# Kernel optimization log

Hardware: AMD Instinct MI355X
Metric: run time of the kernel (lower is better)

Reference implementation:

```python
import math
import jax, jax.numpy as jnp
import numpy as np

CHUNK_LEN = 64
NUM_HEADS = 16
HIDDEN = 1024
HEAD = HIDDEN // NUM_HEADS


def setup_inputs() -> dict:
    key = jax.random.key(0)
    ks = jax.random.split(key, 8)
    B, S, C, N, L = 4, 2048, 32, 2, 128
    scale = 1.0 / math.sqrt(HIDDEN)
    return {
        "query": jax.random.normal(ks[0], (B, S, HIDDEN), jnp.float32),
        "kv": jax.random.normal(ks[1], (B, C, N, L, HIDDEN), jnp.float32),
        "Wq": jax.random.normal(ks[2], (HIDDEN, HIDDEN), jnp.float32) * scale,
        "bq": jnp.zeros((HIDDEN,), jnp.float32),
        "Wk": jax.random.normal(ks[3], (HIDDEN, HIDDEN), jnp.float32) * scale,
        "bk": jnp.zeros((HIDDEN,), jnp.float32),
        "Wv": jax.random.normal(ks[4], (HIDDEN, HIDDEN), jnp.float32) * scale,
        "bv": jnp.zeros((HIDDEN,), jnp.float32),
    }


def reference(query, kv, Wq, bq, Wk, bk, Wv, bv):
    B, S, H = query.shape
    _, C, N, L, _ = kv.shape
    # shift query right by chunk_len-1 and pad to n_chunks*chunk_len
    q = query[:, CHUNK_LEN - 1:]
    add_len = C * CHUNK_LEN - q.shape[1]
    q = jnp.pad(q, ((0, 0), (0, add_len), (0, 0)))
    q = q.reshape(B, C, CHUNK_LEN, H)
    q = (q @ Wq.T + bq).reshape(B, C, CHUNK_LEN, NUM_HEADS, HEAD)
    k = (kv @ Wk.T + bk).reshape(B, C, N, L, NUM_HEADS, HEAD)
    v = (kv @ Wv.T + bv).reshape(B, C, N, L, NUM_HEADS, HEAD)
    # scores: [B, C, heads, chunk_len, N, L]
    attn = jnp.einsum("bcihd,bcnjhd->bchinj", q, k) / math.sqrt(HEAD)
    # softmax over flattened neighbor dims (n, j)
    attn = jax.nn.softmax(attn.reshape(B, C, NUM_HEADS, CHUNK_LEN, N * L), axis=-1)
    attn = attn.reshape(B, C, NUM_HEADS, CHUNK_LEN, N, L)
    h = jnp.einsum("bchinj,bcnjhd->bcihd", attn, v).reshape(B, C * CHUNK_LEN, H)
    # shift left: prepend chunk_len-1 zeros, truncate to seq_len
    h = jnp.pad(h, ((0, 0), (CHUNK_LEN - 1, 0), (0, 0)))[:, :S]
    return h
```

## Files before the change

### kernel.cpp

```cpp
#include <hip/hip_runtime.h>
#include <stdint.h>

#define HD 1024
#define SEQ 2048
#define NC 32

typedef __bf16 bf16x4 __attribute__((ext_vector_type(4)));
typedef __bf16 bf16x8 __attribute__((ext_vector_type(8)));
typedef float f32x4 __attribute__((ext_vector_type(4)));

__device__ inline unsigned short f2bf(float f) {
  union { float f; unsigned int u; } v; v.f = f;
  unsigned int r = v.u + 0x7fffu + ((v.u >> 16) & 1u);
  return (unsigned short)(r >> 16);
}
__device__ inline unsigned int pk2bf(float a, float b) {
  return (unsigned int)f2bf(a) | ((unsigned int)f2bf(b) << 16);
}
__device__ inline bf16x8 ld_frag8(const unsigned short* p) {
  bf16x4 lo = *(const bf16x4*)p;
  bf16x4 hi = *(const bf16x4*)(p + 4);
  return __builtin_shufflevector(lo, hi, 0, 1, 2, 3, 4, 5, 6, 7);
}
__device__ inline void glds16(const unsigned short* g, unsigned short* l) {
  __builtin_amdgcn_global_load_lds(
      (const __attribute__((address_space(1))) unsigned int*)g,
      (__attribute__((address_space(3))) unsigned int*)l, 16, 0, 0);
}
__device__ inline int2 swz_bid() {
  int lin = blockIdx.y * 8 + blockIdx.x;
  int s = (lin & 7) * (int)gridDim.y + (lin >> 3);
  return make_int2(s & 7, s >> 3);
}
__device__ inline int swz64(int row, int j) { return (row * 8 + (j ^ (row & 7))) * 8; }
__device__ inline int swz32(int row, int j) {
  int lr8 = row >> 1;
  return (lr8 * 8 + ((((row & 1) << 2) | j) ^ (lr8 & 7))) * 8;
}

__global__ __launch_bounds__(256) void zero_head_kernel(float* __restrict__ out) {
  int i = (blockIdx.x * 256 + threadIdx.x) * 4;
  int b = i / 64512;
  int r = i - b * 64512;
  *(float4*)(out + (size_t)b * (SEQ * HD) + r) = make_float4(0.f, 0.f, 0.f, 0.f);
}

__global__ __launch_bounds__(256) void prep_q_kernel(const float* __restrict__ q,
                                                     unsigned short* __restrict__ out,
                                                     float* __restrict__ oz) {
  int bid = blockIdx.x;
  if (bid < 252) {
    int i = (bid * 256 + threadIdx.x) * 4;
    int b = i / 64512;
    int r = i - b * 64512;
    *(float4*)(oz + (size_t)b * (SEQ * HD) + r) = make_float4(0.f, 0.f, 0.f, 0.f);
    return;
  }
  int i = (bid - 252) * 256 + threadIdx.x;
  int g = i >> 7, c8 = (i & 127) * 8;
  int b = g >> 11, tt = g & 2047;
  uint4 o = make_uint4(0, 0, 0, 0);
  if (tt < 1985) {
    const float* src = q + ((size_t)(b << 11) + tt + 63) * HD + c8;
    float4 a = *(const float4*)src;
    float4 bb = *(const float4*)(src + 4);
    o = make_uint4(pk2bf(a.x, a.y), pk2bf(a.z, a.w), pk2bf(bb.x, bb.y), pk2bf(bb.z, bb.w));
  }
  *(uint4*)(out + (size_t)g * HD + c8) = o;
}

__global__ __launch_bounds__(256) void cvt_kernel(const float* __restrict__ in,
                                                  unsigned short* __restrict__ out, int n8) {
  int i = blockIdx.x * 256 + threadIdx.x;
  if (i < n8) {
    float4 a = ((const float4*)in)[(size_t)i * 2];
    float4 b = ((const float4*)in)[(size_t)i * 2 + 1];
    ((uint4*)out)[i] = make_uint4(pk2bf(a.x, a.y), pk2bf(a.z, a.w),
                                  pk2bf(b.x, b.y), pk2bf(b.z, b.w));
  }
}

__global__ __launch_bounds__(256) void cvt_w3_kernel(const float* __restrict__ Wq,
                                                     const float* __restrict__ Wk,
                                                     const float* __restrict__ Wv,
                                                     unsigned short* __restrict__ dst) {
  int bid = blockIdx.x;
  int which = bid >> 9;
  int i = (bid & 511) * 256 + threadIdx.x;
  const float* src = which == 0 ? Wq : (which == 1 ? Wk : Wv);
  float4 a = ((const float4*)src)[(size_t)i * 2];
  float4 b = ((const float4*)src)[(size_t)i * 2 + 1];
  ((uint4*)(dst + (size_t)which * 1048576))[i] =
      make_uint4(pk2bf(a.x, a.y), pk2bf(a.z, a.w), pk2bf(b.x, b.y), pk2bf(b.z, b.w));
}

__global__ __launch_bounds__(256, 2) void gemm_q_kernel(
    const unsigned short* __restrict__ A, const unsigned short* __restrict__ W,
    const float* __restrict__ bias, unsigned short* __restrict__ Cout) {
  __shared__ unsigned short lds_a[128 * 64];
  __shared__ unsigned short lds_b[128 * 64];
  const int t = threadIdx.x;
  const int l = t & 63, w = t >> 6;
  const int wm = w >> 1, wn = w & 1;
  const int lr = l & 15, lq = l >> 4;
  const int2 bid = swz_bid();
  const size_t arow0 = (size_t)bid.y * 128;
  const size_t brow0 = (size_t)bid.x * 128;
  int pr[4], pco[4];
#pragma unroll
  for (int p = 0; p < 4; ++p) {
    int pc = p * 256 + t;
    pr[p] = pc >> 3;
    pco[p] = ((pc & 7) ^ (pr[p] & 7)) * 8;
  }

  f32x4 acc[4][4];
  for (int i = 0; i < 4; i++)
    for (int j = 0; j < 4; j++) acc[i][j] = (f32x4){0.f, 0.f, 0.f, 0.f};

  for (int kk = 0; kk < 16; ++kk) {
    const int k0 = kk * 64;
    __syncthreads();
#pragma unroll
    for (int p = 0; p < 4; ++p) {
      glds16(A + (arow0 + pr[p]) * HD + k0 + pco[p], lds_a + (p * 256 + t) * 8);
      glds16(W + (brow0 + pr[p]) * HD + k0 + pco[p], lds_b + (p * 256 + t) * 8);
    }
    __syncthreads();
#pragma unroll
    for (int h = 0; h < 2; ++h) {
      bf16x8 af[4], bfr[4];
      for (int mt = 0; mt < 4; ++mt)
        af[mt] = *(const bf16x8*)(lds_a + swz64(wm * 64 + mt * 16 + lr, h * 4 + lq));
      for (int nt = 0; nt < 4; ++nt)
        bfr[nt] = *(const bf16x8*)(lds_b + swz64(wn * 64 + nt * 16 + lr, h * 4 + lq));
      for (int mt = 0; mt < 4; ++mt)
        for (int nt = 0; nt < 4; ++nt)
          acc[mt][nt] = __builtin_amdgcn_mfma_f32_16x16x32_bf16(af[mt], bfr[nt], acc[mt][nt], 0, 0, 0);
    }
  }

  for (int nt = 0; nt < 4; ++nt) {
    int n = bid.x * 128 + wn * 64 + nt * 16 + lr;
    float bvv = bias[n];
    for (int mt = 0; mt < 4; ++mt) {
      size_t mbase = arow0 + wm * 64 + mt * 16 + lq * 4;
      for (int r = 0; r < 4; ++r)
        Cout[(mbase + r) * HD + n] = f2bf(acc[mt][nt][r] + bvv);
    }
  }
}

__global__ __launch_bounds__(256, 2) void gemm_kv_kernel(
    const unsigned short* __restrict__ A, const unsigned short* __restrict__ Wk,
    const unsigned short* __restrict__ Wv, const float* __restrict__ bk,
    const float* __restrict__ bv, unsigned short* __restrict__ Kout,
    unsigned short* __restrict__ Vt) {
  __shared__ unsigned short lds_a[2][128 * 32];
  __shared__ unsigned short lds_k[2][128 * 32];
  __shared__ unsigned short lds_v[2][128 * 32];
  const int t = threadIdx.x;
  const int l = t & 63, w = t >> 6;
  const int wm = w >> 1, wn = w & 1;
  const int lr = l & 15, lq = l >> 4;
  const int2 bid = swz_bid();
  const size_t arow0 = (size_t)bid.y * 128;
  const size_t brow0 = (size_t)bid.x * 128;
  int pr[2], pco[2];
#pragma unroll
  for (int p = 0; p < 2; ++p) {
    int pc = p * 256 + t;
    int lr8 = pc >> 3;
    int e = (pc & 7) ^ (lr8 & 7);
    pr[p] = lr8 * 2 + (e >> 2);
    pco[p] = (e & 3) * 8;
  }

  f32x4 acck[4][4], accv[4][4];
  for (int i = 0; i < 4; i++)
    for (int j = 0; j < 4; j++) {
      acck[i][j] = (f32x4){0.f, 0.f, 0.f, 0.f};
      accv[i][j] = (f32x4){0.f, 0.f, 0.f, 0.f};
    }

  auto stage = [&](int buf, int k0) {
#pragma unroll
    for (int p = 0; p < 2; ++p) {
      glds16(A + (arow0 + pr[p]) * HD + k0 + pco[p], lds_a[buf] + (p * 256 + t) * 8);
      glds16(Wk + (brow0 + pr[p]) * HD + k0 + pco[p], lds_k[buf] + (p * 256 + t) * 8);
      glds16(Wv + (brow0 + pr[p]) * HD + k0 + pco[p], lds_v[buf] + (p * 256 + t) * 8);
    }
  };
  auto compute = [&](int buf) {
    bf16x8 af[4];
    for (int mt = 0; mt < 4; ++mt)
      af[mt] = *(const bf16x8*)(lds_a[buf] + swz32(wm * 64 + mt * 16 + lr, lq));
    {
      bf16x8 bfr[4];
      for (int nt = 0; nt < 4; ++nt)
        bfr[nt] = *(const bf16x8*)(lds_k[buf] + swz32(wn * 64 + nt * 16 + lr, lq));
      for (int mt = 0; mt < 4; ++mt)
        for (int nt = 0; nt < 4; ++nt)
          acck[mt][nt] = __builtin_amdgcn_mfma_f32_16x16x32_bf16(af[mt], bfr[nt], acck[mt][nt], 0, 0, 0);
    }
    {
      bf16x8 bfr[4];
      for (int nt = 0; nt < 4; ++nt)
        bfr[nt] = *(const bf16x8*)(lds_v[buf] + swz32(wn * 64 + nt * 16 + lr, lq));
      for (int mt = 0; mt < 4; ++mt)
        for (int nt = 0; nt < 4; ++nt)
          accv[mt][nt] = __builtin_amdgcn_mfma_f32_16x16x32_bf16(af[mt], bfr[nt], accv[mt][nt], 0, 0, 0);
    }
  };

  stage(0, 0);
  for (int kk = 0; kk < 31; ++kk) {
    const int cur = kk & 1;
    stage(cur ^ 1, (kk + 1) * 32);
    asm volatile("s_waitcnt vmcnt(6)" ::: "memory");
    __builtin_amdgcn_s_barrier();
    compute(cur);
    __builtin_amdgcn_s_barrier();
  }
  asm volatile("s_waitcnt vmcnt(0)" ::: "memory");
  __builtin_amdgcn_s_barrier();
  compute(1);

  for (int nt = 0; nt < 4; ++nt) {
    int n = bid.x * 128 + wn * 64 + nt * 16 + lr;
    float bvv = bk[n];
    for (int mt = 0; mt < 4; ++mt) {
      size_t mbase = arow0 + wm * 64 + mt * 16 + lq * 4;
      for (int r = 0; r < 4; ++r)
        Kout[(mbase + r) * HD + n] = f2bf(acck[mt][nt][r] + bvv);
    }
  }
  for (int nt = 0; nt < 4; ++nt) {
    int n = bid.x * 128 + wn * 64 + nt * 16 + lr;
    float bvv = bv[n];
    int h = n >> 6, d = n & 63;
    for (int mt = 0; mt < 4; ++mt) {
      size_t m0 = arow0 + wm * 64 + mt * 16 + lq * 4;
      size_t bc = m0 >> 8, j = m0 & 255;
      *(ushort4*)(Vt + ((bc * 16 + h) * 64 + d) * 256 + j) =
          make_ushort4(f2bf(accv[mt][nt][0] + bvv), f2bf(accv[mt][nt][1] + bvv),
                       f2bf(accv[mt][nt][2] + bvv), f2bf(accv[mt][nt][3] + bvv));
    }
  }
}

__global__ __launch_bounds__(256, 2) void gemm_f32_kernel(
    const float* __restrict__ A, const float* __restrict__ W,
    const float* __restrict__ bias, unsigned short* __restrict__ Cout,
    int store_vt, int qremap) {
  __shared__ unsigned short lds_a[128 * 32];
  __shared__ unsigned short lds_b[128 * 32];
  const int t = threadIdx.x;
  const int l = t & 63, w = t >> 6;
  const int wm = w >> 1, wn = w & 1;
  const int lr = l & 15, lq = l >> 4;
  const size_t arow0 = (size_t)blockIdx.y * 128;
  const size_t brow0 = (size_t)blockIdx.x * 128;

  f32x4 acc[4][4];
  for (int i = 0; i < 4; i++)
    for (int j = 0; j < 4; j++) acc[i][j] = (f32x4){0.f, 0.f, 0.f, 0.f};

  for (int kk = 0; kk < 32; ++kk) {
    const int k0 = kk * 32;
    uint4 av[2], bv[2];
    for (int p = 0; p < 2; ++p) {
      int chunk = p * 256 + t;
      int row = chunk >> 2, c8 = (chunk & 3) * 8;
      size_t grow = arow0 + row;
      bool valid = true;
      const float* srcA;
      if (qremap) {
        int bb = (int)(grow >> 11), tt = (int)(grow & 2047);
        valid = tt < 1985;
        srcA = A + ((size_t)(bb << 11) + tt + 63) * HD + k0 + c8;
      } else {
        srcA = A + grow * HD + k0 + c8;
      }
      if (valid) {
        float4 x = *(const float4*)srcA, y = *(const float4*)(srcA + 4);
        av[p] = make_uint4(pk2bf(x.x, x.y), pk2bf(x.z, x.w), pk2bf(y.x, y.y), pk2bf(y.z, y.w));
      } else av[p] = make_uint4(0, 0, 0, 0);
      const float* srcB = W + (brow0 + row) * HD + k0 + c8;
      float4 x = *(const float4*)srcB, y = *(const float4*)(srcB + 4);
      bv[p] = make_uint4(pk2bf(x.x, x.y), pk2bf(x.z, x.w), pk2bf(y.y, y.y), pk2bf(y.z, y.w));
    }
    for (int p = 0; p < 2; ++p) {
      int chunk = p * 256 + t;
      int row = chunk >> 2, c8 = (chunk & 3) * 8;
      const float* srcB = W + (brow0 + row) * HD + k0 + c8;
      float4 x = *(const float4*)srcB, y = *(const float4*)(srcB + 4);
      bv[p] = make_uint4(pk2bf(x.x, x.y), pk2bf(x.z, x.w), pk2bf(y.x, y.y), pk2bf(y.z, y.w));
    }
    __syncthreads();
    for (int p = 0; p < 2; ++p) {
      int chunk = p * 256 + t;
      *(uint4*)(lds_a + chunk * 8) = av[p];
      *(uint4*)(lds_b + chunk * 8) = bv[p];
    }
    __syncthreads();
    bf16x8 af[4], bfr[4];
    for (int mt = 0; mt < 4; ++mt)
      af[mt] = *(const bf16x8*)(lds_a + (wm * 64 + mt * 16 + lr) * 32 + lq * 8);
    for (int nt = 0; nt < 4; ++nt)
      bfr[nt] = *(const bf16x8*)(lds_b + (wn * 64 + nt * 16 + lr) * 32 + lq * 8);
    for (int mt = 0; mt < 4; ++mt)
      for (int nt = 0; nt < 4; ++nt)
        acc[mt][nt] = __builtin_amdgcn_mfma_f32_16x16x32_bf16(af[mt], bfr[nt], acc[mt][nt], 0, 0, 0);
  }

  if (!store_vt) {
    for (int nt = 0; nt < 4; ++nt) {
      int n = blockIdx.x * 128 + wn * 64 + nt * 16 + lr;
      float bvv = bias[n];
      for (int mt = 0; mt < 4; ++mt) {
        size_t mbase = arow0 + wm * 64 + mt * 16 + lq * 4;
        for (int r = 0; r < 4; ++r)
          Cout[(mbase + r) * HD + n] = f2bf(acc[mt][nt][r] + bvv);
      }
    }
  } else {
    for (int nt = 0; nt < 4; ++nt) {
      int n = blockIdx.x * 128 + wn * 64 + nt * 16 + lr;
      float bvv = bias[n];
      int h = n >> 6, d = n & 63;
      for (int mt = 0; mt < 4; ++mt) {
        size_t m0 = arow0 + wm * 64 + mt * 16 + lq * 4;
        size_t bc = m0 >> 8, j = m0 & 255;
        *(ushort4*)(Cout + ((bc * 16 + h) * 64 + d) * 256 + j) =
            make_ushort4(f2bf(acc[mt][nt][0] + bvv), f2bf(acc[mt][nt][1] + bvv),
                         f2bf(acc[mt][nt][2] + bvv), f2bf(acc[mt][nt][3] + bvv));
      }
    }
  }
}

#define QK_STRIDE 72
#define P_STRIDE 260

__global__ __launch_bounds__(256, 3) void attn_kernel(
    const unsigned short* __restrict__ Qp, const unsigned short* __restrict__ Kp,
    const unsigned short* __restrict__ Vt, float* __restrict__ out) {
  __shared__ unsigned short k_s[256 * QK_STRIDE];
  const int t = threadIdx.x;
  const int l = t & 63, w = t >> 6;
  const int lr = l & 15, lq = l >> 4;
  const int bid = blockIdx.x;
  const int head = bid & 15, cc = (bid >> 4) & 31, b = bid >> 9;
  const size_t qrow0 = (size_t)(b * NC + cc) * 64;
  const size_t kvrow0 = (size_t)(b * NC + cc) * 256;
  const int hcol = head * 64;
  const unsigned short* vbase = Vt + ((size_t)((b * NC + cc) * 16 + head) * 64) * 256;

  for (int p = 0; p < 8; ++p) {
    int chunk = p * 256 + t;
    int row = chunk >> 3, c8 = (chunk & 7) * 8;
    *(uint4*)(k_s + row * QK_STRIDE + c8) = *(const uint4*)(Kp + (kvrow0 + row) * HD + hcol + c8);
  }
  bf16x8 qa0 = ld_frag8(Qp + (qrow0 + w * 16 + lr) * HD + hcol + lq * 8);
  bf16x8 qa1 = ld_frag8(Qp + (qrow0 + w * 16 + lr) * HD + hcol + 32 + lq * 8);
  __syncthreads();

  f32x4 sc[16];
  __builtin_amdgcn_s_setprio(1);
  for (int nt = 0; nt < 16; ++nt) {
    bf16x8 kb0 = ld_frag8(k_s + (nt * 16 + lr) * QK_STRIDE + lq * 8);
    bf16x8 kb1 = ld_frag8(k_s + (nt * 16 + lr) * QK_STRIDE + 32 + lq * 8);
    f32x4 a = (f32x4){0.f, 0.f, 0.f, 0.f};
    a = __builtin_amdgcn_mfma_f32_16x16x32_bf16(kb0, qa0, a, 0, 0, 0);
    a = __builtin_amdgcn_mfma_f32_16x16x32_bf16(kb1, qa1, a, 0, 0, 0);
    sc[nt] = a;
  }
  __builtin_amdgcn_s_setprio(0);

  float m = -1e30f;
  for (int nt = 0; nt < 16; ++nt)
    for (int r = 0; r < 4; ++r) m = fmaxf(m, sc[nt][r]);
  m = fmaxf(m, __shfl_xor(m, 16));
  m = fmaxf(m, __shfl_xor(m, 32));
  float s = 0.f;
  const float cexp = 0.18033688011112042f;
  for (int nt = 0; nt < 16; ++nt)
    for (int r = 0; r < 4; ++r) {
      float p = exp2f((sc[nt][r] - m) * cexp);
      sc[nt][r] = p;
      s += p;
    }
  s += __shfl_xor(s, 16);
  s += __shfl_xor(s, 32);

  bf16x8 va[4];
#pragma unroll
  for (int nt2 = 0; nt2 < 4; ++nt2)
    va[nt2] = *(const bf16x8*)(vbase + (size_t)(nt2 * 16 + lr) * 256 + lq * 8);

  __syncthreads();

  for (int nt = 0; nt < 16; ++nt) {
    *(uint2*)(k_s + (w * 16 + lr) * P_STRIDE + nt * 16 + lq * 4) =
        make_uint2(pk2bf(sc[nt][0], sc[nt][1]), pk2bf(sc[nt][2], sc[nt][3]));
  }

  f32x4 o[4];
  for (int i = 0; i < 4; ++i) o[i] = (f32x4){0.f, 0.f, 0.f, 0.f};
  bf16x8 vbuf[4];
#pragma unroll
  for (int ks = 0; ks < 8; ks += 2) {
#pragma unroll
    for (int nt2 = 0; nt2 < 4; ++nt2)
      vbuf[nt2] = *(const bf16x8*)(vbase + (size_t)(nt2 * 16 + lr) * 256 + (ks + 1) * 32 + lq * 8);
    bf16x8 pa = ld_frag8(k_s + (w * 16 + lr) * P_STRIDE + ks * 32 + lq * 8);
    __builtin_amdgcn_s_setprio(1);
#pragma unroll
    for (int nt2 = 0; nt2 < 4; ++nt2)
      o[nt2] = __builtin_amdgcn_mfma_f32_16x16x32_bf16(pa, va[nt2], o[nt2], 0, 0, 0);
    __builtin_amdgcn_s_setprio(0);
    if (ks + 2 < 8) {
#pragma unroll
      for (int nt2 = 0; nt2 < 4; ++nt2)
        va[nt2] = *(const bf16x8*)(vbase + (size_t)(nt2 * 16 + lr) * 256 + (ks + 2) * 32 + lq * 8);
    }
    bf16x8 pb = ld_frag8(k_s + (w * 16 + lr) * P_STRIDE + (ks + 1) * 32 + lq * 8);
    __builtin_amdgcn_s_setprio(1);
#pragma unroll
    for (int nt2 = 0; nt2 < 4; ++nt2)
      o[nt2] = __builtin_amdgcn_mfma_f32_16x16x32_bf16(pb, vbuf[nt2], o[nt2], 0, 0, 0);
    __builtin_amdgcn_s_setprio(0);
  }

  for (int r = 0; r < 4; ++r) {
    int strip = w * 16 + lq * 4 + r;
    int trow = cc * 64 + strip;
    float sv = __shfl(s, lq * 4 + r, 16);
    if (trow < 1985) {
      size_t orow = (size_t)b * SEQ + trow + 63;
      float inv = 1.0f / sv;
      for (int nt2 = 0; nt2 < 4; ++nt2)
        out[orow * HD + hcol + nt2 * 16 + lr] = o[nt2][r] * inv;
    }
  }
}

extern "C" void kernel_launch(void* const* d_in, const int* in_sizes, int n_in,
                              void* d_out, int out_size, void* d_ws, size_t ws_size,
                              hipStream_t stream) {
  (void)in_sizes; (void)n_in; (void)out_size;
  const float* query = (const float*)d_in[0];
  const float* kv    = (const float*)d_in[1];
  const float* Wq    = (const float*)d_in[2];
  const float* bq    = (const float*)d_in[3];
  const float* Wk    = (const float*)d_in[4];
  const float* bk    = (const float*)d_in[5];
  const float* Wv    = (const float*)d_in[6];
  const float* bv    = (const float*)d_in[7];
  float* out = (float*)d_out;

  unsigned short* Qp  = (unsigned short*)d_ws;
  unsigned short* Kp  = Qp + (size_t)8192 * 1024;
  unsigned short* Vt  = Kp + (size_t)32768 * 1024;
  unsigned short* Qbf = Vt + (size_t)32768 * 1024;
  unsigned short* KVb = Qbf + (size_t)8192 * 1024;
  unsigned short* Wqb = KVb + (size_t)32768 * 1024;
  const size_t need = ((size_t)8192 * 1024 * 2 + (size_t)32768 * 1024 * 2 + (size_t)1024 * 1024 * 3) * 2;
  const bool big = ws_size >= need;

  if (big) {
    prep_q_kernel<<<dim3(4348), dim3(256), 0, stream>>>(query, Qbf, out);
    cvt_w3_kernel<<<dim3(1536), dim3(256), 0, stream>>>(Wq, Wk, Wv, Wqb);
    cvt_kernel<<<dim3(16384), dim3(256), 0, stream>>>(kv, KVb, 4194304);
    gemm_q_kernel<<<dim3(8, 64), dim3(256), 0, stream>>>(Qbf, Wqb, bq, Qp);
    gemm_kv_kernel<<<dim3(8, 256), dim3(256), 0, stream>>>(KVb, Wqb + (size_t)1048576,
                                                           Wqb + (size_t)2097152, bk, bv, Kp, Vt);
  } else {
    zero_head_kernel<<<dim3(252), dim3(256), 0, stream>>>(out);
    gemm_f32_kernel<<<dim3(8, 64), dim3(256), 0, stream>>>(query, Wq, bq, Qp, 0, 1);
    gemm_f32_kernel<<<dim3(8, 256), dim3(256), 0, stream>>>(kv, Wk, bk, Kp, 0, 0);
    gemm_f32_kernel<<<dim3(8, 256), dim3(256), 0, stream>>>(kv, Wv, bv, Vt, 1, 0);
  }
  attn_kernel<<<dim3(2048), dim3(256), 0, stream>>>(Qp, Kp, Vt, out);
}
```

Baseline: 466.9 us.

## Merge conversion kernels and Q/KV projection GEMMs into single launches

```diff
diff --git a/kernel.cpp b/kernel.cpp
--- a/kernel.cpp
+++ b/kernel.cpp
@@ -27,16 +27,7 @@
       (const __attribute__((address_space(1))) unsigned int*)g,
       (__attribute__((address_space(3))) unsigned int*)l, 16, 0, 0);
 }
-__device__ inline int2 swz_bid() {
-  int lin = blockIdx.y * 8 + blockIdx.x;
-  int s = (lin & 7) * (int)gridDim.y + (lin >> 3);
-  return make_int2(s & 7, s >> 3);
-}
 __device__ inline int swz64(int row, int j) { return (row * 8 + (j ^ (row & 7))) * 8; }
-__device__ inline int swz32(int row, int j) {
-  int lr8 = row >> 1;
-  return (lr8 * 8 + ((((row & 1) << 2) | j) ^ (lr8 & 7))) * 8;
-}
 
 __global__ __launch_bounds__(256) void zero_head_kernel(float* __restrict__ out) {
   int i = (blockIdx.x * 256 + threadIdx.x) * 4;
@@ -45,67 +36,67 @@
   *(float4*)(out + (size_t)b * (SEQ * HD) + r) = make_float4(0.f, 0.f, 0.f, 0.f);
 }
 
-__global__ __launch_bounds__(256) void prep_q_kernel(const float* __restrict__ q,
-                                                     unsigned short* __restrict__ out,
-                                                     float* __restrict__ oz) {
+__global__ __launch_bounds__(256) void prep_all_kernel(
+    const float* __restrict__ query, const float* __restrict__ kv,
+    const float* __restrict__ Wq, const float* __restrict__ Wk,
+    const float* __restrict__ Wv, unsigned short* __restrict__ Qbf,
+    unsigned short* __restrict__ KVb, unsigned short* __restrict__ Wb,
+    float* __restrict__ oz) {
   int bid = blockIdx.x;
-  if (bid < 252) {
-    int i = (bid * 256 + threadIdx.x) * 4;
-    int b = i / 64512;
-    int r = i - b * 64512;
-    *(float4*)(oz + (size_t)b * (SEQ * HD) + r) = make_float4(0.f, 0.f, 0.f, 0.f);
+  if (bid < 16384) {
+    int i = bid * 256 + threadIdx.x;
+    float4 a = ((const float4*)kv)[(size_t)i * 2];
+    float4 b = ((const float4*)kv)[(size_t)i * 2 + 1];
+    ((uint4*)KVb)[i] = make_uint4(pk2bf(a.x, a.y), pk2bf(a.z, a.w),
+                                  pk2bf(b.x, b.y), pk2bf(b.z, b.w));
     return;
   }
-  int i = (bid - 252) * 256 + threadIdx.x;
-  int g = i >> 7, c8 = (i & 127) * 8;
-  int b = g >> 11, tt = g & 2047;
-  uint4 o = make_uint4(0, 0, 0, 0);
-  if (tt < 1985) {
-    const float* src = q + ((size_t)(b << 11) + tt + 63) * HD + c8;
-    float4 a = *(const float4*)src;
-    float4 bb = *(const float4*)(src + 4);
-    o = make_uint4(pk2bf(a.x, a.y), pk2bf(a.z, a.w), pk2bf(bb.x, bb.y), pk2bf(bb.z, bb.w));
-  }
-  *(uint4*)(out + (size_t)g * HD + c8) = o;
-}
-
-__global__ __launch_bounds__(256) void cvt_kernel(const float* __restrict__ in,
-                                                  unsigned short* __restrict__ out, int n8) {
-  int i = blockIdx.x * 256 + threadIdx.x;
-  if (i < n8) {
-    float4 a = ((const float4*)in)[(size_t)i * 2];
-    float4 b = ((const float4*)in)[(size_t)i * 2 + 1];
-    ((uint4*)out)[i] = make_uint4(pk2bf(a.x, a.y), pk2bf(a.z, a.w),
-                                  pk2bf(b.x, b.y), pk2bf(b.z, b.w));
-  }
-}
-
-__global__ __launch_bounds__(256) void cvt_w3_kernel(const float* __restrict__ Wq,
-                                                     const float* __restrict__ Wk,
-                                                     const float* __restrict__ Wv,
-                                                     unsigned short* __restrict__ dst) {
-  int bid = blockIdx.x;
-  int which = bid >> 9;
-  int i = (bid & 511) * 256 + threadIdx.x;
-  const float* src = which == 0 ? Wq : (which == 1 ? Wk : Wv);
-  float4 a = ((const float4*)src)[(size_t)i * 2];
-  float4 b = ((const float4*)src)[(size_t)i * 2 + 1];
-  ((uint4*)(dst + (size_t)which * 1048576))[i] =
-      make_uint4(pk2bf(a.x, a.y), pk2bf(a.z, a.w), pk2bf(b.x, b.y), pk2bf(b.z, b.w));
-}
-
-__global__ __launch_bounds__(256, 2) void gemm_q_kernel(
-    const unsigned short* __restrict__ A, const unsigned short* __restrict__ W,
-    const float* __restrict__ bias, unsigned short* __restrict__ Cout) {
+  bid -= 16384;
+  if (bid < 4096) {
+    int i = bid * 256 + threadIdx.x;
+    int g = i >> 7, c8 = (i & 127) * 8;
+    int b = g >> 11, tt = g & 2047;
+    uint4 o = make_uint4(0, 0, 0, 0);
+    if (tt < 1985) {
+      const float* src = query + ((size_t)(b << 11) + tt + 63) * HD + c8;
+      float4 a = *(const float4*)src;
+      float4 bb = *(const float4*)(src + 4);
+      o = make_uint4(pk2bf(a.x, a.y), pk2bf(a.z, a.w), pk2bf(bb.x, bb.y), pk2bf(bb.z, bb.w));
+    }
+    *(uint4*)(Qbf + (size_t)g * HD + c8) = o;
+    return;
+  }
+  bid -= 4096;
+  if (bid < 1536) {
+    int which = bid >> 9;
+    int i = (bid & 511) * 256 + threadIdx.x;
+    const float* src = which == 0 ? Wq : (which == 1 ? Wk : Wv);
+    float4 a = ((const float4*)src)[(size_t)i * 2];
+    float4 b = ((const float4*)src)[(size_t)i * 2 + 1];
+    ((uint4*)(Wb + (size_t)which * 1048576))[i] =
+        make_uint4(pk2bf(a.x, a.y), pk2bf(a.z, a.w), pk2bf(b.x, b.y), pk2bf(b.z, b.w));
+    return;
+  }
+  bid -= 1536;
+  int i = (bid * 256 + threadIdx.x) * 4;
+  int b = i / 64512;
+  int r = i - b * 64512;
+  *(float4*)(oz + (size_t)b * (SEQ * HD) + r) = make_float4(0.f, 0.f, 0.f, 0.f);
+}
+
+__global__ __launch_bounds__(256, 2) void gemm_all_kernel(
+    const unsigned short* __restrict__ Qbf, const unsigned short* __restrict__ KVb,
+    const unsigned short* __restrict__ Wb,
+    const float* __restrict__ bq, const float* __restrict__ bk, const float* __restrict__ bv,
+    unsigned short* __restrict__ Qp, unsigned short* __restrict__ Kp,
+    unsigned short* __restrict__ Vt) {
   __shared__ unsigned short lds_a[128 * 64];
   __shared__ unsigned short lds_b[128 * 64];
+  __shared__ unsigned short lds_c[128 * 64];
   const int t = threadIdx.x;
   const int l = t & 63, w = t >> 6;
   const int wm = w >> 1, wn = w & 1;
   const int lr = l & 15, lq = l >> 4;
-  const int2 bid = swz_bid();
-  const size_t arow0 = (size_t)bid.y * 128;
-  const size_t brow0 = (size_t)bid.x * 128;
   int pr[4], pco[4];
 #pragma unroll
   for (int p = 0; p < 4; ++p) {
@@ -114,137 +105,118 @@
     pco[p] = ((pc & 7) ^ (pr[p] & 7)) * 8;
   }
 
-  f32x4 acc[4][4];
-  for (int i = 0; i < 4; i++)
-    for (int j = 0; j < 4; j++) acc[i][j] = (f32x4){0.f, 0.f, 0.f, 0.f};
-
-  for (int kk = 0; kk < 16; ++kk) {
-    const int k0 = kk * 64;
-    __syncthreads();
-#pragma unroll
-    for (int p = 0; p < 4; ++p) {
-      glds16(A + (arow0 + pr[p]) * HD + k0 + pco[p], lds_a + (p * 256 + t) * 8);
-      glds16(W + (brow0 + pr[p]) * HD + k0 + pco[p], lds_b + (p * 256 + t) * 8);
-    }
-    __syncthreads();
-#pragma unroll
-    for (int h = 0; h < 2; ++h) {
-      bf16x8 af[4], bfr[4];
-      for (int mt = 0; mt < 4; ++mt)
-        af[mt] = *(const bf16x8*)(lds_a + swz64(wm * 64 + mt * 16 + lr, h * 4 + lq));
-      for (int nt = 0; nt < 4; ++nt)
-        bfr[nt] = *(const bf16x8*)(lds_b + swz64(wn * 64 + nt * 16 + lr, h * 4 + lq));
-      for (int mt = 0; mt < 4; ++mt)
+  if (blockIdx.y < 256) {
+    int lin = blockIdx.y * 8 + blockIdx.x;
+    int s = (lin & 7) * 256 + (lin >> 3);
+    const int bx = s & 7, by = s >> 3;
+    const size_t arow0 = (size_t)by * 128;
+    const size_t brow0 = (size_t)bx * 128;
+    const unsigned short* Wk = Wb + (size_t)1048576;
+    const unsigned short* Wv = Wb + (size_t)2097152;
+
+    f32x4 acck[4][4], accv[4][4];
+    for (int i = 0; i < 4; i++)
+      for (int j = 0; j < 4; j++) {
+        acck[i][j] = (f32x4){0.f, 0.f, 0.f, 0.f};
+        accv[i][j] = (f32x4){0.f, 0.f, 0.f, 0.f};
+      }
+
+    for (int kk = 0; kk < 16; ++kk) {
+      const int k0 = kk * 64;
+      __syncthreads();
+#pragma unroll
+      for (int p = 0; p < 4; ++p) {
+        glds16(KVb + (arow0 + pr[p]) * HD + k0 + pco[p], lds_a + (p * 256 + t) * 8);
+        glds16(Wk + (brow0 + pr[p]) * HD + k0 + pco[p], lds_b + (p * 256 + t) * 8);
+        glds16(Wv + (brow0 + pr[p]) * HD + k0 + pco[p], lds_c + (p * 256 + t) * 8);
+      }
+      __syncthreads();
+#pragma unroll
+      for (int h = 0; h < 2; ++h) {
+        bf16x8 af[4];
+        for (int mt = 0; mt < 4; ++mt)
+          af[mt] = *(const bf16x8*)(lds_a + swz64(wm * 64 + mt * 16 + lr, h * 4 + lq));
+        {
+          bf16x8 bfr[4];
+          for (int nt = 0; nt < 4; ++nt)
+            bfr[nt] = *(const bf16x8*)(lds_b + swz64(wn * 64 + nt * 16 + lr, h * 4 + lq));
+          for (int mt = 0; mt < 4; ++mt)
+            for (int nt = 0; nt < 4; ++nt)
+              acck[mt][nt] = __builtin_amdgcn_mfma_f32_16x16x32_bf16(af[mt], bfr[nt], acck[mt][nt], 0, 0, 0);
+        }
+        {
+          bf16x8 bfr[4];
+          for (int nt = 0; nt < 4; ++nt)
+            bfr[nt] = *(const bf16x8*)(lds_c + swz64(wn * 64 + nt * 16 + lr, h * 4 + lq));
+          for (int mt = 0; mt < 4; ++mt)
+            for (int nt = 0; nt < 4; ++nt)
+              accv[mt][nt] = __builtin_amdgcn_mfma_f32_16x16x32_bf16(af[mt], bfr[nt], accv[mt][nt], 0, 0, 0);
+        }
+      }
+    }
+
+    for (int nt = 0; nt < 4; ++nt) {
+      int n = bx * 128 + wn * 64 + nt * 16 + lr;
+      float bvv = bk[n];
+      for (int mt = 0; mt < 4; ++mt) {
+        size_t mbase = arow0 + wm * 64 + mt * 16 + lq * 4;
+        for (int r = 0; r < 4; ++r)
+          Kp[(mbase + r) * HD + n] = f2bf(acck[mt][nt][r] + bvv);
+      }
+    }
+    for (int nt = 0; nt < 4; ++nt) {
+      int n = bx * 128 + wn * 64 + nt * 16 + lr;
+      float bvv = bv[n];
+      int h = n >> 6, d = n & 63;
+      for (int mt = 0; mt < 4; ++mt) {
+        size_t m0 = arow0 + wm * 64 + mt * 16 + lq * 4;
+        size_t bc = m0 >> 8, j = m0 & 255;
+        *(ushort4*)(Vt + ((bc * 16 + h) * 64 + d) * 256 + j) =
+            make_ushort4(f2bf(accv[mt][nt][0] + bvv), f2bf(accv[mt][nt][1] + bvv),
+                         f2bf(accv[mt][nt][2] + bvv), f2bf(accv[mt][nt][3] + bvv));
+      }
+    }
+  } else {
+    int lin = (blockIdx.y - 256) * 8 + blockIdx.x;
+    int s = (lin & 7) * 64 + (lin >> 3);
+    const int bx = s & 7, by = s >> 3;
+    const size_t arow0 = (size_t)by * 128;
+    const size_t brow0 = (size_t)bx * 128;
+
+    f32x4 acc[4][4];
+    for (int i = 0; i < 4; i++)
+      for (int j = 0; j < 4; j++) acc[i][j] = (f32x4){0.f, 0.f, 0.f, 0.f};
+
+    for (int kk = 0; kk < 16; ++kk) {
+      const int k0 = kk * 64;
+      __syncthreads();
+#pragma unroll
+      for (int p = 0; p < 4; ++p) {
+        glds16(Qbf + (arow0 + pr[p]) * HD + k0 + pco[p], lds_a + (p * 256 + t) * 8);
+        glds16(Wb + (brow0 + pr[p]) * HD + k0 + pco[p], lds_b + (p * 256 + t) * 8);
+      }
+      __syncthreads();
+#pragma unroll
+      for (int h = 0; h < 2; ++h) {
+        bf16x8 af[4], bfr[4];
+        for (int mt = 0; mt < 4; ++mt)
+          af[mt] = *(const bf16x8*)(lds_a + swz64(wm * 64 + mt * 16 + lr, h * 4 + lq));
         for (int nt = 0; nt < 4; ++nt)
-          acc[mt][nt] = __builtin_amdgcn_mfma_f32_16x16x32_bf16(af[mt], bfr[nt], acc[mt][nt], 0, 0, 0);
-    }
-  }
-
-  for (int nt = 0; nt < 4; ++nt) {
-    int n = bid.x * 128 + wn * 64 + nt * 16 + lr;
-    float bvv = bias[n];
-    for (int mt = 0; mt < 4; ++mt) {
-      size_t mbase = arow0 + wm * 64 + mt * 16 + lq * 4;
-      for (int r = 0; r < 4; ++r)
-        Cout[(mbase + r) * HD + n] = f2bf(acc[mt][nt][r] + bvv);
-    }
-  }
-}
-
-__global__ __launch_bounds__(256, 2) void gemm_kv_kernel(
-    const unsigned short* __restrict__ A, const unsigned short* __restrict__ Wk,
-    const unsigned short* __restrict__ Wv, const float* __restrict__ bk,
-    const float* __restrict__ bv, unsigned short* __restrict__ Kout,
-    unsigned short* __restrict__ Vt) {
-  __shared__ unsigned short lds_a[2][128 * 32];
-  __shared__ unsigned short lds_k[2][128 * 32];
-  __shared__ unsigned short lds_v[2][128 * 32];
-  const int t = threadIdx.x;
-  const int l = t & 63, w = t >> 6;
-  const int wm = w >> 1, wn = w & 1;
-  const int lr = l & 15, lq = l >> 4;
-  const int2 bid = swz_bid();
-  const size_t arow0 = (size_t)bid.y * 128;
-  const size_t brow0 = (size_t)bid.x * 128;
-  int pr[2], pco[2];
-#pragma unroll
-  for (int p = 0; p < 2; ++p) {
-    int pc = p * 256 + t;
-    int lr8 = pc >> 3;
-    int e = (pc & 7) ^ (lr8 & 7);
-    pr[p] = lr8 * 2 + (e >> 2);
-    pco[p] = (e & 3) * 8;
-  }
-
-  f32x4 acck[4][4], accv[4][4];
-  for (int i = 0; i < 4; i++)
-    for (int j = 0; j < 4; j++) {
-      acck[i][j] = (f32x4){0.f, 0.f, 0.f, 0.f};
-      accv[i][j] = (f32x4){0.f, 0.f, 0.f, 0.f};
-    }
-
-  auto stage = [&](int buf, int k0) {
-#pragma unroll
-    for (int p = 0; p < 2; ++p) {
-      glds16(A + (arow0 + pr[p]) * HD + k0 + pco[p], lds_a[buf] + (p * 256 + t) * 8);
-      glds16(Wk + (brow0 + pr[p]) * HD + k0 + pco[p], lds_k[buf] + (p * 256 + t) * 8);
-      glds16(Wv + (brow0 + pr[p]) * HD + k0 + pco[p], lds_v[buf] + (p * 256 + t) * 8);
-    }
-  };
-  auto compute = [&](int buf) {
-    bf16x8 af[4];
-    for (int mt = 0; mt < 4; ++mt)
-      af[mt] = *(const bf16x8*)(lds_a[buf] + swz32(wm * 64 + mt * 16 + lr, lq));
-    {
-      bf16x8 bfr[4];
-      for (int nt = 0; nt < 4; ++nt)
-        bfr[nt] = *(const bf16x8*)(lds_k[buf] + swz32(wn * 64 + nt * 16 + lr, lq));
-      for (int mt = 0; mt < 4; ++mt)
-        for (int nt = 0; nt < 4; ++nt)
-          acck[mt][nt] = __builtin_amdgcn_mfma_f32_16x16x32_bf16(af[mt], bfr[nt], acck[mt][nt], 0, 0, 0);
-    }
-    {
-      bf16x8 bfr[4];
-      for (int nt = 0; nt < 4; ++nt)
-        bfr[nt] = *(const bf16x8*)(lds_v[buf] + swz32(wn * 64 + nt * 16 + lr, lq));
-      for (int mt = 0; mt < 4; ++mt)
-        for (int nt = 0; nt < 4; ++nt)
-          accv[mt][nt] = __builtin_amdgcn_mfma_f32_16x16x32_bf16(af[mt], bfr[nt], accv[mt][nt], 0, 0, 0);
-    }
-  };
-
-  stage(0, 0);
-  for (int kk = 0; kk < 31; ++kk) {
-    const int cur = kk & 1;
-    stage(cur ^ 1, (kk + 1) * 32);
-    asm volatile("s_waitcnt vmcnt(6)" ::: "memory");
-    __builtin_amdgcn_s_barrier();
-    compute(cur);
-    __builtin_amdgcn_s_barrier();
-  }
-  asm volatile("s_waitcnt vmcnt(0)" ::: "memory");
-  __builtin_amdgcn_s_barrier();
-  compute(1);
-
-  for (int nt = 0; nt < 4; ++nt) {
-    int n = bid.x * 128 + wn * 64 + nt * 16 + lr;
-    float bvv = bk[n];
-    for (int mt = 0; mt < 4; ++mt) {
-      size_t mbase = arow0 + wm * 64 + mt * 16 + lq * 4;
-      for (int r = 0; r < 4; ++r)
-        Kout[(mbase + r) * HD + n] = f2bf(acck[mt][nt][r] + bvv);
-    }
-  }
-  for (int nt = 0; nt < 4; ++nt) {
-    int n = bid.x * 128 + wn * 64 + nt * 16 + lr;
-    float bvv = bv[n];
-    int h = n >> 6, d = n & 63;
-    for (int mt = 0; mt < 4; ++mt) {
-      size_t m0 = arow0 + wm * 64 + mt * 16 + lq * 4;
-      size_t bc = m0 >> 8, j = m0 & 255;
-      *(ushort4*)(Vt + ((bc * 16 + h) * 64 + d) * 256 + j) =
-          make_ushort4(f2bf(accv[mt][nt][0] + bvv), f2bf(accv[mt][nt][1] + bvv),
-                       f2bf(accv[mt][nt][2] + bvv), f2bf(accv[mt][nt][3] + bvv));
+          bfr[nt] = *(const bf16x8*)(lds_b + swz64(wn * 64 + nt * 16 + lr, h * 4 + lq));
+        for (int mt = 0; mt < 4; ++mt)
+          for (int nt = 0; nt < 4; ++nt)
+            acc[mt][nt] = __builtin_amdgcn_mfma_f32_16x16x32_bf16(af[mt], bfr[nt], acc[mt][nt], 0, 0, 0);
+      }
+    }
+
+    for (int nt = 0; nt < 4; ++nt) {
+      int n = bx * 128 + wn * 64 + nt * 16 + lr;
+      float bvv = bq[n];
+      for (int mt = 0; mt < 4; ++mt) {
+        size_t mbase = arow0 + wm * 64 + mt * 16 + lq * 4;
+        for (int r = 0; r < 4; ++r)
+          Qp[(mbase + r) * HD + n] = f2bf(acc[mt][nt][r] + bvv);
+      }
     }
   }
 }
@@ -288,13 +260,6 @@
       } else av[p] = make_uint4(0, 0, 0, 0);
       const float* srcB = W + (brow0 + row) * HD + k0 + c8;
       float4 x = *(const float4*)srcB, y = *(const float4*)(srcB + 4);
-      bv[p] = make_uint4(pk2bf(x.x, x.y), pk2bf(x.z, x.w), pk2bf(y.y, y.y), pk2bf(y.z, y.w));
-    }
-    for (int p = 0; p < 2; ++p) {
-      int chunk = p * 256 + t;
-      int row = chunk >> 2, c8 = (chunk & 3) * 8;
-      const float* srcB = W + (brow0 + row) * HD + k0 + c8;
-      float4 x = *(const float4*)srcB, y = *(const float4*)(srcB + 4);
       bv[p] = make_uint4(pk2bf(x.x, x.y), pk2bf(x.z, x.w), pk2bf(y.x, y.y), pk2bf(y.z, y.w));
     }
     __syncthreads();
@@ -470,12 +435,10 @@
   const bool big = ws_size >= need;
 
   if (big) {
-    prep_q_kernel<<<dim3(4348), dim3(256), 0, stream>>>(query, Qbf, out);
-    cvt_w3_kernel<<<dim3(1536), dim3(256), 0, stream>>>(Wq, Wk, Wv, Wqb);
-    cvt_kernel<<<dim3(16384), dim3(256), 0, stream>>>(kv, KVb, 4194304);
-    gemm_q_kernel<<<dim3(8, 64), dim3(256), 0, stream>>>(Qbf, Wqb, bq, Qp);
-    gemm_kv_kernel<<<dim3(8, 256), dim3(256), 0, stream>>>(KVb, Wqb + (size_t)1048576,
-                                                           Wqb + (size_t)2097152, bk, bv, Kp, Vt);
+    prep_all_kernel<<<dim3(22268), dim3(256), 0, stream>>>(query, kv, Wq, Wk, Wv,
+                                                           Qbf, KVb, Wqb, out);
+    gemm_all_kernel<<<dim3(8, 320), dim3(256), 0, stream>>>(Qbf, KVb, Wqb, bq, bk, bv,
+                                                            Qp, Kp, Vt);
   } else {
     zero_head_kernel<<<dim3(252), dim3(256), 0, stream>>>(out);
     gemm_f32_kernel<<<dim3(8, 64), dim3(256), 0, stream>>>(query, Wq, bq, Qp, 0, 1);
```

Result: no change. 461.5 us (-1.2%).
